# Optimization experiments

Measured on AMD Instinct MI355X. Metric: run time of the kernel, lower is better.

## Reference

```python
import jax, jax.numpy as jnp
from jax import lax
import numpy as np

BETA = 0.9
THR1 = 1.0
THR2 = 0.8


def setup_inputs() -> dict:
    key = jax.random.key(0)
    ks = jax.random.split(key, 10)
    B, T, I, H, O = 256, 100, 1024, 2048, 1024
    x = jax.random.uniform(ks[0], (B, T, I), dtype=jnp.float32)
    cd1 = jax.random.normal(ks[1], (I,), dtype=jnp.float32) * 0.01
    v1 = jnp.array([0.5], dtype=jnp.float32)
    cd2 = jax.random.normal(ks[2], (H,), dtype=jnp.float32) * 0.01
    v2 = jnp.array([0.5], dtype=jnp.float32)
    W1 = jax.random.normal(ks[3], (H, I), dtype=jnp.float32) * 0.02
    b1 = jnp.zeros((H,), dtype=jnp.float32)
    W2 = jax.random.normal(ks[4], (O, H), dtype=jnp.float32) * 0.02
    b2 = jnp.zeros((O,), dtype=jnp.float32)
    out_scale = jnp.ones((O,), dtype=jnp.float32)
    out_bias = jnp.zeros((O,), dtype=jnp.float32)
    return {"x": x, "cd1": cd1, "v1": v1, "cd2": cd2, "v2": v2,
            "W1": W1, "b1": b1, "W2": W2, "b2": b2,
            "out_scale": out_scale, "out_bias": out_bias}


def _lif(inp, pot, cd, v, thr):
    # relativistic delay-weighted LIF step; inp/pot: [B, N]
    vc = jnp.clip(v, 0.0, 0.999)[0]
    gamma = 1.0 / jnp.sqrt(1.0 - vc * vc)
    delay_factors = jnp.exp(-(gamma * jnp.abs(cd) * vc))  # [N]
    new_pot = pot * BETA + inp * delay_factors
    spk = (new_pot > thr).astype(inp.dtype)
    return spk, new_pot * (1.0 - spk)


def reference(x, cd1, v1, cd2, v2, W1, b1, W2, b2, out_scale, out_bias):
    B, T, I = x.shape
    H = cd2.shape[0]
    xt = jnp.swapaxes(x, 0, 1)  # [T, B, I]

    def step(carry, x_t):
        p1, p2 = carry
        s1, p1 = _lif(x_t, p1, cd1, v1, THR1)
        h = s1 @ W1.T + b1  # [B, H]
        s2, p2 = _lif(h, p2, cd2, v2, THR2)
        o = s2 @ W2.T + b2  # [B, O]
        return (p1, p2), o

    init = (jnp.zeros((B, I), x.dtype), jnp.zeros((B, H), x.dtype))
    _, outs = lax.scan(step, init, xt)  # [T, B, O]

    vc = jnp.clip(v1, 0.0, 0.999)[0]
    gamma = 1.0 / jnp.sqrt(1.0 - vc * vc)
    t = jnp.arange(T, dtype=x.dtype)
    tw = jnp.exp(-(gamma - 1.0) * t)
    tw = tw / tw.sum()
    weighted = jnp.einsum('tbo,t->bo', outs, tw)
    return weighted * out_scale + out_bias
```

## Files before the change

### kernel.cpp

```cpp
#include <hip/hip_runtime.h>
#include <hip/hip_bf16.h>
#include <math.h>

#define BETA_F 0.9f
#define THR1_F 1.0f
#define THR2_F 0.8f

typedef __attribute__((ext_vector_type(8))) short bf16x8;
typedef __attribute__((ext_vector_type(4))) float f32x4;

__device__ __forceinline__ void gload_lds16(const void* g, void* l) {
    __builtin_amdgcn_global_load_lds(
        (const __attribute__((address_space(1))) void*)g,
        (__attribute__((address_space(3))) void*)l, 16, 0, 0);
}

__device__ __forceinline__ ushort f2bf(float f) {
    __hip_bfloat16 h = __float2bfloat16(f);
    return *(ushort*)&h;
}
__device__ __forceinline__ float bf2f(ushort u) {
    __hip_bfloat16 h;
    *(ushort*)&h = u;
    return __bfloat162float(h);
}

__global__ void k_init(const float* __restrict__ cd1, const float* __restrict__ v1,
                       const float* __restrict__ cd2, const float* __restrict__ v2,
                       float* __restrict__ df1, float* __restrict__ df2,
                       float* __restrict__ p1, float* __restrict__ p2,
                       float* __restrict__ acc2,
                       int I, int H, int BI, int BH) {
    float vc1 = fminf(fmaxf(v1[0], 0.0f), 0.999f);
    float vc2 = fminf(fmaxf(v2[0], 0.0f), 0.999f);
    double g1 = 1.0 / sqrt(1.0 - (double)vc1 * (double)vc1);
    double g2 = 1.0 / sqrt(1.0 - (double)vc2 * (double)vc2);
    int total = I + H + BI + BH + BH;
    for (int idx = blockIdx.x * blockDim.x + threadIdx.x; idx < total;
         idx += gridDim.x * blockDim.x) {
        if (idx < I) {
            df1[idx] = (float)exp(-(g1 * fabs((double)cd1[idx]) * (double)vc1));
        } else if (idx < I + H) {
            int j = idx - I;
            df2[j] = (float)exp(-(g2 * fabs((double)cd2[j]) * (double)vc2));
        } else if (idx < I + H + BI) {
            p1[idx - I - H] = 0.0f;
        } else if (idx < I + H + BI + BH) {
            p2[idx - I - H - BI] = 0.0f;
        } else {
            acc2[idx - I - H - BI - BH] = 0.0f;
        }
    }
}

__global__ void k_tw(const float* __restrict__ v1, float* __restrict__ tw, int T) {
    __shared__ float sh[256];
    float vc = fminf(fmaxf(v1[0], 0.0f), 0.999f);
    double g = 1.0 / sqrt(1.0 - (double)vc * (double)vc);
    int t = threadIdx.x;
    float val = 0.0f;
    if (t < T) val = (float)exp(-(g - 1.0) * (double)t);
    sh[t] = val;
    __syncthreads();
    for (int s = 128; s > 0; s >>= 1) {
        if (t < s) sh[t] += sh[t + s];
        __syncthreads();
    }
    float sum = sh[0];
    if (t < T) tw[t] = val / sum;
}

__global__ void k_wsplit(const float* __restrict__ W, ushort* __restrict__ hi,
                         ushort* __restrict__ lo, int n) {
    int i = blockIdx.x * blockDim.x + threadIdx.x;
    if (i >= n) return;
    float w = W[i];
    ushort h = f2bf(w);
    float hf = bf2f(h);
    ushort l = f2bf(w - hf);
    hi[i] = h;
    lo[i] = l;
}

__global__ void k_lif1(const float* __restrict__ x, const float* __restrict__ df1,
                       float* __restrict__ p1, ushort* __restrict__ s1,
                       int Bsz, int T, int I, int t0, int TC) {
    int idx = blockIdx.x * blockDim.x + threadIdx.x;
    if (idx >= Bsz * I) return;
    int b = idx / I;
    int i = idx - b * I;
    float df = df1[i];
    float p = p1[idx];
    const float* xp = x + ((size_t)b * T + t0) * I + i;
    size_t strideS = (size_t)Bsz * I;
    for (int t = 0; t < TC; ++t) {
        float xv = xp[(size_t)t * I];
        float pn = __fadd_rn(__fmul_rn(p, BETA_F), __fmul_rn(xv, df));
        bool spk = pn > THR1_F;
        s1[(size_t)t * strideS + idx] = spk ? (ushort)0x3F80 : (ushort)0;
        p = spk ? 0.0f : pn;
    }
    p1[idx] = p;
}

__global__ void k_lif2(const float* __restrict__ h, const float* __restrict__ df2,
                       const float* __restrict__ tw, float* __restrict__ p2,
                       float* __restrict__ acc2, int Bsz, int H, int t0, int TC) {
    int idx = blockIdx.x * blockDim.x + threadIdx.x;
    if (idx >= Bsz * H) return;
    int j = idx % H;
    float df = df2[j];
    float p = p2[idx];
    float acc = acc2[idx];
    size_t strideH = (size_t)Bsz * H;
    for (int t = 0; t < TC; ++t) {
        float hv = h[(size_t)t * strideH + idx];
        float pn = __fadd_rn(__fmul_rn(p, BETA_F), __fmul_rn(hv, df));
        bool spk = pn > THR2_F;
        if (spk) acc += tw[t0 + t];
        p = spk ? 0.0f : pn;
    }
    p2[idx] = p;
    acc2[idx] = acc;
}

__global__ __launch_bounds__(256)
void k_gemm_mfma(const ushort* __restrict__ A, const ushort* __restrict__ Bhi,
                 const ushort* __restrict__ Blo, const float* __restrict__ bias,
                 float* __restrict__ C, int N, int K, int gx) {
    __shared__ ushort As[128 * 32];
    __shared__ ushort Bh[128 * 32];
    __shared__ ushort Bl[128 * 32];
    int nwg = gridDim.x;
    int lin = blockIdx.x;
    int cpx = nwg >> 3;
    int swz = (lin & 7) * cpx + (lin >> 3);
    int bx = swz % gx, by = swz / gx;
    int mBase = by * 128, nBase = bx * 128;
    int tid = threadIdx.x;
    int wid = tid >> 6, lane = tid & 63;

    int srow = tid >> 2;
    int scol = (tid & 3) * 8;
    const ushort* aS0 = A + (size_t)(mBase + srow) * K + scol;
    const ushort* aS1 = A + (size_t)(mBase + 64 + srow) * K + scol;
    const ushort* bhS0 = Bhi + (size_t)(nBase + srow) * K + scol;
    const ushort* bhS1 = Bhi + (size_t)(nBase + 64 + srow) * K + scol;
    const ushort* blS0 = Blo + (size_t)(nBase + srow) * K + scol;
    const ushort* blS1 = Blo + (size_t)(nBase + 64 + srow) * K + scol;
    ushort* aD0 = As + wid * 512;
    ushort* aD1 = As + 2048 + wid * 512;
    ushort* bhD0 = Bh + wid * 512;
    ushort* bhD1 = Bh + 2048 + wid * 512;
    ushort* blD0 = Bl + wid * 512;
    ushort* blD1 = Bl + 2048 + wid * 512;

    int wr = wid >> 1, wc = wid & 1;
    int aoff = (wr * 64 + (lane & 15)) * 32 + (lane >> 4) * 8;
    int boff = (wc * 64 + (lane & 15)) * 32 + (lane >> 4) * 8;

    f32x4 acc[4][4];
#pragma unroll
    for (int i = 0; i < 4; i++)
#pragma unroll
        for (int j = 0; j < 4; j++) acc[i][j] = (f32x4)(0.0f);

    for (int k0 = 0; k0 < K; k0 += 32) {
        __syncthreads();
        gload_lds16(aS0 + k0, aD0);
        gload_lds16(aS1 + k0, aD1);
        gload_lds16(bhS0 + k0, bhD0);
        gload_lds16(bhS1 + k0, bhD1);
        gload_lds16(blS0 + k0, blD0);
        gload_lds16(blS1 + k0, blD1);
        __syncthreads();
        bf16x8 af[4], bhf[4], blf[4];
#pragma unroll
        for (int f = 0; f < 4; f++) {
            af[f] = *(const bf16x8*)&As[aoff + f * 16 * 32];
            bhf[f] = *(const bf16x8*)&Bh[boff + f * 16 * 32];
            blf[f] = *(const bf16x8*)&Bl[boff + f * 16 * 32];
        }
#pragma unroll
        for (int i = 0; i < 4; i++)
#pragma unroll
            for (int j = 0; j < 4; j++) {
                acc[i][j] = __builtin_amdgcn_mfma_f32_16x16x32_bf16(
                    af[i], bhf[j], acc[i][j], 0, 0, 0);
                acc[i][j] = __builtin_amdgcn_mfma_f32_16x16x32_bf16(
                    af[i], blf[j], acc[i][j], 0, 0, 0);
            }
    }
    int crow0 = mBase + wr * 64 + (lane >> 4) * 4;
    int ccol0 = nBase + wc * 64 + (lane & 15);
#pragma unroll
    for (int i = 0; i < 4; i++) {
#pragma unroll
        for (int j = 0; j < 4; j++) {
            int col = ccol0 + j * 16;
            float bv = bias[col];
#pragma unroll
            for (int r = 0; r < 4; r++) {
                int row = crow0 + i * 16 + r;
                C[(size_t)row * N + col] = acc[i][j][r] + bv;
            }
        }
    }
}

__global__ __launch_bounds__(256)
void k_gemm64(const float* __restrict__ A, const float* __restrict__ Bm,
              float* __restrict__ P, int M, int N, int K, int KS) {
    __shared__ float As[16][68];
    __shared__ float Bs[16][68];
    int tid = threadIdx.x;
    int mBase = blockIdx.y * 64, nBase = blockIdx.x * 64;
    int k0 = blockIdx.z * KS;
    int lr = tid >> 2, lk = (tid & 3) * 4;
    int ty = tid >> 4, tx = tid & 15;
    float acc[4][4];
#pragma unroll
    for (int i = 0; i < 4; i++)
#pragma unroll
        for (int j = 0; j < 4; j++) acc[i][j] = 0.0f;
    const float* Ap = A + (size_t)(mBase + lr) * K + k0 + lk;
    const float* Bp = Bm + (size_t)(nBase + lr) * K + k0 + lk;
    for (int k = 0; k < KS; k += 16) {
        float4 av = *(const float4*)(Ap + k);
        float4 bv = *(const float4*)(Bp + k);
        __syncthreads();
        As[lk + 0][lr] = av.x; As[lk + 1][lr] = av.y;
        As[lk + 2][lr] = av.z; As[lk + 3][lr] = av.w;
        Bs[lk + 0][lr] = bv.x; Bs[lk + 1][lr] = bv.y;
        Bs[lk + 2][lr] = bv.z; Bs[lk + 3][lr] = bv.w;
        __syncthreads();
#pragma unroll
        for (int kk = 0; kk < 16; ++kk) {
            float4 a4 = *(const float4*)&As[kk][ty * 4];
            float4 b4 = *(const float4*)&Bs[kk][tx * 4];
            float aa[4] = {a4.x, a4.y, a4.z, a4.w};
            float bb[4] = {b4.x, b4.y, b4.z, b4.w};
#pragma unroll
            for (int i = 0; i < 4; i++)
#pragma unroll
                for (int j = 0; j < 4; j++)
                    acc[i][j] = fmaf(aa[i], bb[j], acc[i][j]);
        }
    }
#pragma unroll
    for (int i = 0; i < 4; i++)
#pragma unroll
        for (int j = 0; j < 4; j++)
            P[((size_t)blockIdx.z * M + mBase + ty * 4 + i) * N + nBase + tx * 4 + j] =
                acc[i][j];
}

__global__ void k_fin(const float* __restrict__ P, const float* __restrict__ b2,
                      const float* __restrict__ scale, const float* __restrict__ bias2,
                      float* __restrict__ out, int M, int N, int Z) {
    int i = blockIdx.x * blockDim.x + threadIdx.x;
    if (i >= M * N) return;
    float s = 0.0f;
    for (int z = 0; z < Z; ++z) s += P[(size_t)z * M * N + i];
    int col = i % N;
    out[i] = (s + b2[col]) * scale[col] + bias2[col];
}

extern "C" void kernel_launch(void* const* d_in, const int* in_sizes, int n_in,
                              void* d_out, int out_size, void* d_ws, size_t ws_size,
                              hipStream_t stream) {
    const float* x = (const float*)d_in[0];
    const float* cd1 = (const float*)d_in[1];
    const float* v1 = (const float*)d_in[2];
    const float* cd2 = (const float*)d_in[3];
    const float* v2 = (const float*)d_in[4];
    const float* W1 = (const float*)d_in[5];
    const float* b1 = (const float*)d_in[6];
    const float* W2 = (const float*)d_in[7];
    const float* b2 = (const float*)d_in[8];
    const float* out_scale = (const float*)d_in[9];
    const float* out_bias = (const float*)d_in[10];

    int I = in_sizes[1];
    int H = in_sizes[3];
    int O = in_sizes[8];
    int Bsz = out_size / O;
    int T = in_sizes[0] / (Bsz * I);
    const int ZSPLIT = 4;

    float* ws = (float*)d_ws;
    size_t off = 0;
    auto alloc = [&](size_t n) {
        size_t cur = off;
        off += (n + 63) & ~(size_t)63;
        return cur;
    };
    size_t o_df1 = alloc(I);
    size_t o_df2 = alloc(H);
    size_t o_tw = alloc(T);
    size_t o_p1 = alloc((size_t)Bsz * I);
    size_t o_p2 = alloc((size_t)Bsz * H);
    size_t o_acc2 = alloc((size_t)Bsz * H);
    size_t o_whi = alloc((size_t)H * I / 2);
    size_t o_wlo = alloc((size_t)H * I / 2);
    size_t o_part = alloc((size_t)ZSPLIT * Bsz * O);
    size_t persist = off;

    size_t wsFloats = ws_size / 4;
    size_t perStep = (size_t)Bsz * I / 2 + (size_t)Bsz * H + 128;
    int TC = 1;
    if (wsFloats > persist) {
        size_t tcMax = (wsFloats - persist) / perStep;
        TC = (int)(tcMax < (size_t)T ? tcMax : (size_t)T);
        if (TC < 1) TC = 1;
    }
    size_t o_s1 = alloc(((size_t)TC * Bsz * I + 1) / 2);
    size_t o_h = alloc((size_t)TC * Bsz * H);

    float* df1 = ws + o_df1;
    float* df2 = ws + o_df2;
    float* tw = ws + o_tw;
    float* p1 = ws + o_p1;
    float* p2 = ws + o_p2;
    float* acc2 = ws + o_acc2;
    ushort* whi = (ushort*)(ws + o_whi);
    ushort* wlo = (ushort*)(ws + o_wlo);
    float* part = ws + o_part;
    ushort* s1c = (ushort*)(ws + o_s1);
    float* hbuf = ws + o_h;

    k_init<<<2048, 256, 0, stream>>>(cd1, v1, cd2, v2, df1, df2, p1, p2, acc2, I, H,
                                     Bsz * I, Bsz * H);
    k_tw<<<1, 256, 0, stream>>>(v1, tw, T);
    k_wsplit<<<(H * I + 255) / 256, 256, 0, stream>>>(W1, whi, wlo, H * I);

    for (int t0 = 0; t0 < T; t0 += TC) {
        int tc = (T - t0 < TC) ? (T - t0) : TC;
        k_lif1<<<(Bsz * I + 255) / 256, 256, 0, stream>>>(x, df1, p1, s1c, Bsz, T, I,
                                                          t0, tc);
        int Mrows = tc * Bsz;
        int gx = H / 128;
        int nwg = (Mrows / 128) * gx;
        k_gemm_mfma<<<nwg, 256, 0, stream>>>(s1c, whi, wlo, b1, hbuf, H, I, gx);
        k_lif2<<<(Bsz * H + 255) / 256, 256, 0, stream>>>(hbuf, df2, tw, p2, acc2,
                                                          Bsz, H, t0, tc);
    }
    dim3 g2(O / 64, Bsz / 64, ZSPLIT);
    k_gemm64<<<g2, 256, 0, stream>>>(acc2, W2, part, Bsz, O, H, H / ZSPLIT);
    k_fin<<<(Bsz * O + 255) / 256, 256, 0, stream>>>(part, b2, out_scale, out_bias,
                                                     (float*)d_out, Bsz, O, ZSPLIT);
}
```

Measured before the change: 555.1 us.

## Double-buffer MFMA GEMM LDS tiles with 256x128 blocks and swizzled layout

The spike-by-W1 MFMA GEMM now uses 512-thread blocks covering 256x128 output tiles. LDS tiles are double-buffered so the next K-slice's global-to-LDS loads overlap the current slice's MFMAs, which removes one barrier per iteration. An XOR swizzle on the 16-byte chunk index is meant to cut LDS bank conflicts, and s_setprio raises wave priority around the MFMA bursts. LDS use roughly triples per block, which may limit occupancy, and the launch now requires Mrows to be divisible by 256.

```diff
diff --git a/kernel.cpp b/kernel.cpp
--- a/kernel.cpp
+++ b/kernel.cpp
@@ -124,40 +124,35 @@
     acc2[idx] = acc;
 }
 
-__global__ __launch_bounds__(256)
+__global__ __launch_bounds__(512, 4)
 void k_gemm_mfma(const ushort* __restrict__ A, const ushort* __restrict__ Bhi,
                  const ushort* __restrict__ Blo, const float* __restrict__ bias,
                  float* __restrict__ C, int N, int K, int gx) {
-    __shared__ ushort As[128 * 32];
-    __shared__ ushort Bh[128 * 32];
-    __shared__ ushort Bl[128 * 32];
+    __shared__ ushort As[2][8192];
+    __shared__ ushort Bh[2][4096];
+    __shared__ ushort Bl[2][4096];
     int nwg = gridDim.x;
     int lin = blockIdx.x;
     int cpx = nwg >> 3;
     int swz = (lin & 7) * cpx + (lin >> 3);
     int bx = swz % gx, by = swz / gx;
-    int mBase = by * 128, nBase = bx * 128;
+    int mBase = by * 256, nBase = bx * 128;
     int tid = threadIdx.x;
     int wid = tid >> 6, lane = tid & 63;
 
     int srow = tid >> 2;
-    int scol = (tid & 3) * 8;
-    const ushort* aS0 = A + (size_t)(mBase + srow) * K + scol;
-    const ushort* aS1 = A + (size_t)(mBase + 64 + srow) * K + scol;
-    const ushort* bhS0 = Bhi + (size_t)(nBase + srow) * K + scol;
-    const ushort* bhS1 = Bhi + (size_t)(nBase + 64 + srow) * K + scol;
-    const ushort* blS0 = Blo + (size_t)(nBase + srow) * K + scol;
-    const ushort* blS1 = Blo + (size_t)(nBase + 64 + srow) * K + scol;
-    ushort* aD0 = As + wid * 512;
-    ushort* aD1 = As + 2048 + wid * 512;
-    ushort* bhD0 = Bh + wid * 512;
-    ushort* bhD1 = Bh + 2048 + wid * 512;
-    ushort* blD0 = Bl + wid * 512;
-    ushort* blD1 = Bl + 2048 + wid * 512;
+    int schunk = (tid & 3) ^ ((tid >> 3) & 3);
+    const ushort* aS0 = A + (size_t)(mBase + srow) * K + schunk * 8;
+    const ushort* aS1 = A + (size_t)(mBase + 128 + srow) * K + schunk * 8;
+    const ushort* bhS = Bhi + (size_t)(nBase + srow) * K + schunk * 8;
+    const ushort* blS = Blo + (size_t)(nBase + srow) * K + schunk * 8;
 
     int wr = wid >> 1, wc = wid & 1;
-    int aoff = (wr * 64 + (lane & 15)) * 32 + (lane >> 4) * 8;
-    int boff = (wc * 64 + (lane & 15)) * 32 + (lane >> 4) * 8;
+    int l15 = lane & 15;
+    int sw = (l15 >> 1) & 3;
+    int ch = ((lane >> 4) ^ sw) * 8;
+    int aoff = (wr * 64 + l15) * 32 + ch;
+    int boff = (wc * 64 + l15) * 32 + ch;
 
     f32x4 acc[4][4];
 #pragma unroll
@@ -165,34 +160,50 @@
 #pragma unroll
         for (int j = 0; j < 4; j++) acc[i][j] = (f32x4)(0.0f);
 
-    for (int k0 = 0; k0 < K; k0 += 32) {
+    auto stage = [&](int buf, int k0) {
+        gload_lds16(aS0 + k0, &As[buf][tid * 8]);
+        gload_lds16(aS1 + k0, &As[buf][4096 + tid * 8]);
+        gload_lds16(bhS + k0, &Bh[buf][tid * 8]);
+        gload_lds16(blS + k0, &Bl[buf][tid * 8]);
+    };
+    auto compute_tile = [&](int cur) {
+        bf16x8 af[4], bf[4];
+#pragma unroll
+        for (int f = 0; f < 4; f++) af[f] = *(const bf16x8*)&As[cur][aoff + f * 512];
+#pragma unroll
+        for (int f = 0; f < 4; f++) bf[f] = *(const bf16x8*)&Bh[cur][boff + f * 512];
+        __builtin_amdgcn_s_setprio(1);
+#pragma unroll
+        for (int i = 0; i < 4; i++)
+#pragma unroll
+            for (int j = 0; j < 4; j++)
+                acc[i][j] = __builtin_amdgcn_mfma_f32_16x16x32_bf16(af[i], bf[j],
+                                                                    acc[i][j], 0, 0, 0);
+        __builtin_amdgcn_s_setprio(0);
+#pragma unroll
+        for (int f = 0; f < 4; f++) bf[f] = *(const bf16x8*)&Bl[cur][boff + f * 512];
+        __builtin_amdgcn_s_setprio(1);
+#pragma unroll
+        for (int i = 0; i < 4; i++)
+#pragma unroll
+            for (int j = 0; j < 4; j++)
+                acc[i][j] = __builtin_amdgcn_mfma_f32_16x16x32_bf16(af[i], bf[j],
+                                                                    acc[i][j], 0, 0, 0);
+        __builtin_amdgcn_s_setprio(0);
+    };
+
+    int NT = K >> 5;
+    stage(0, 0);
+    __syncthreads();
+    for (int kt = 0; kt < NT - 1; ++kt) {
+        stage((kt + 1) & 1, (kt + 1) << 5);
+        compute_tile(kt & 1);
         __syncthreads();
-        gload_lds16(aS0 + k0, aD0);
-        gload_lds16(aS1 + k0, aD1);
-        gload_lds16(bhS0 + k0, bhD0);
-        gload_lds16(bhS1 + k0, bhD1);
-        gload_lds16(blS0 + k0, blD0);
-        gload_lds16(blS1 + k0, blD1);
-        __syncthreads();
-        bf16x8 af[4], bhf[4], blf[4];
-#pragma unroll
-        for (int f = 0; f < 4; f++) {
-            af[f] = *(const bf16x8*)&As[aoff + f * 16 * 32];
-            bhf[f] = *(const bf16x8*)&Bh[boff + f * 16 * 32];
-            blf[f] = *(const bf16x8*)&Bl[boff + f * 16 * 32];
-        }
-#pragma unroll
-        for (int i = 0; i < 4; i++)
-#pragma unroll
-            for (int j = 0; j < 4; j++) {
-                acc[i][j] = __builtin_amdgcn_mfma_f32_16x16x32_bf16(
-                    af[i], bhf[j], acc[i][j], 0, 0, 0);
-                acc[i][j] = __builtin_amdgcn_mfma_f32_16x16x32_bf16(
-                    af[i], blf[j], acc[i][j], 0, 0, 0);
-            }
-    }
+    }
+    compute_tile((NT - 1) & 1);
+
     int crow0 = mBase + wr * 64 + (lane >> 4) * 4;
-    int ccol0 = nBase + wc * 64 + (lane & 15);
+    int ccol0 = nBase + wc * 64 + l15;
 #pragma unroll
     for (int i = 0; i < 4; i++) {
 #pragma unroll
@@ -340,8 +351,8 @@
                                                           t0, tc);
         int Mrows = tc * Bsz;
         int gx = H / 128;
-        int nwg = (Mrows / 128) * gx;
-        k_gemm_mfma<<<nwg, 256, 0, stream>>>(s1c, whi, wlo, b1, hbuf, H, I, gx);
+        int nwg = (Mrows / 256) * gx;
+        k_gemm_mfma<<<nwg, 512, 0, stream>>>(s1c, whi, wlo, b1, hbuf, H, I, gx);
         k_lif2<<<(Bsz * H + 255) / 256, 256, 0, stream>>>(hbuf, df2, tw, p2, acc2,
                                                           Bsz, H, t0, tc);
     }
```

Measured after the change: 518.5 us. -6.6%, faster.
